# Optimization experiments

Measured on AMD Instinct MI355X. Metric: run time of the kernel, lower is better.

Reference implementation:

```python
import jax, jax.numpy as jnp
import numpy as np

D_MODEL = 1024
N_HEADS = 16
HEAD_DIM = D_MODEL // N_HEADS
B, T = 4, 2048


def setup_inputs() -> dict:
    key = jax.random.key(0)
    k1, k2, k3, k4 = jax.random.split(key, 4)
    x = jax.random.normal(k1, (B, T, D_MODEL), dtype=jnp.float32)
    # bool key-padding mask: True = masked (padded) position
    pad_mask = jax.random.randint(k2, (B, T), 0, 2).astype(jnp.bool_)
    # torch Linear weights: [out_features, in_features], bias=False
    W_qkv = jax.random.normal(k3, (3 * D_MODEL, D_MODEL), dtype=jnp.float32) * (1.0 / np.sqrt(D_MODEL))
    W_proj = jax.random.normal(k4, (D_MODEL, D_MODEL), dtype=jnp.float32) * (1.0 / np.sqrt(D_MODEL))
    return {"x": x, "pad_mask": pad_mask, "W_qkv": W_qkv, "W_proj": W_proj}


def reference(x, pad_mask, W_qkv, W_proj):
    Bv, Tv, C = x.shape
    H, Dh = N_HEADS, HEAD_DIM
    # qkv projection: x @ W_qkv.T -> [B,T,3C], reshape to [B,T,3,H,Dh]
    qkv = jnp.einsum('btc,oc->bto', x, W_qkv).reshape(Bv, Tv, 3, H, Dh)
    q = jnp.transpose(qkv[:, :, 0], (0, 2, 1, 3))  # [B,H,T,Dh]
    k = jnp.transpose(qkv[:, :, 1], (0, 2, 1, 3))
    v = jnp.transpose(qkv[:, :, 2], (0, 2, 1, 3))
    scale = 1.0 / jnp.sqrt(jnp.asarray(Dh, x.dtype))
    attn = jnp.einsum('bhqd,bhkd->bhqk', q, k) * scale  # [B,H,T,T]
    # key-padding mask: broadcast [B,1,1,T]
    attn = jnp.where(pad_mask[:, None, None, :], -jnp.inf, attn)
    attn = jax.nn.softmax(attn, axis=-1)
    out = jnp.einsum('bhqk,bhkd->bhqd', attn, v)  # [B,H,T,Dh]
    out = jnp.transpose(out, (0, 2, 1, 3)).reshape(Bv, Tv, C)
    return jnp.einsum('btc,oc->bto', out, W_proj)
```

## Files before the change

### kernel.cpp

```cpp
#include <hip/hip_runtime.h>
#include <hip/hip_bf16.h>
#include <stdint.h>

typedef __bf16 bf16_t;
typedef __bf16 bf16x8 __attribute__((ext_vector_type(8)));
typedef __bf16 bf16x4 __attribute__((ext_vector_type(4)));
typedef float f32x4 __attribute__((ext_vector_type(4)));

#define DEVFN static __device__ __forceinline__

DEVFN f32x4 mfma16(bf16x8 a, bf16x8 b, f32x4 c) {
  return __builtin_amdgcn_mfma_f32_16x16x32_bf16(a, b, c, 0, 0, 0);
}

#define GLL16(gsrc, ldst) __builtin_amdgcn_global_load_lds( \
    (__attribute__((address_space(1))) void*)(gsrc), \
    (__attribute__((address_space(3))) void*)(ldst), 16, 0, 0)

#define SCALE_Q 0.1803368801111204f

__global__ void prep(const float* __restrict__ x, const float* __restrict__ wqkv,
                     const float* __restrict__ wproj, bf16_t* __restrict__ xb,
                     bf16_t* __restrict__ wqkvb, bf16_t* __restrict__ wprojb,
                     const int* __restrict__ mask, int* __restrict__ tc,
                     int* __restrict__ nk, bf16_t* __restrict__ kb,
                     bf16_t* __restrict__ vtb) {
  const int tid = threadIdx.x;
  if (blockIdx.x < 12288) {
    const int i = blockIdx.x * 256 + tid;
    const float* s;
    bf16_t* d;
    int off;
    if (i < 2097152) { s = x; d = xb; off = i; }
    else if (i < 2097152 + 786432) { s = wqkv; d = wqkvb; off = i - 2097152; }
    else { s = wproj; d = wprojb; off = i - 2883584; }
    f32x4 v = reinterpret_cast<const f32x4*>(s)[off];
    bf16x4 o;
    o[0] = (bf16_t)v[0]; o[1] = (bf16_t)v[1]; o[2] = (bf16_t)v[2]; o[3] = (bf16_t)v[3];
    reinterpret_cast<bf16x4*>(d)[off] = o;
    return;
  }
  const int b = blockIdx.x - 12288;
  const int lane = tid & 63, wv = tid >> 6;
  __shared__ int nk_s;
  const int* mrow = mask + b * 2048;
  if (wv == 0) {
    int base = 0;
    for (int cs = 0; cs < 2048; cs += 64) {
      const int mval = mrow[cs + lane];
      const unsigned long long bal = __ballot(mval == 0);
      const int pre = __popcll(bal & ((1ull << lane) - 1ull));
      if (!mval) tc[b * 2048 + base + pre] = cs + lane;
      base += __popcll(bal);
    }
    if (lane == 0) nk_s = base;
  }
  __syncthreads();
  const int nkb = nk_s;
  if (tid == 0) nk[b] = nkb;
  for (int i = nkb + tid; i < 2048; i += 256) tc[b * 2048 + i] = -1;
  const int ce = (nkb + 63) & ~63;
  for (int hh = wv; hh < 16; hh += 4) {
    const size_t bh = (size_t)(b * 16 + hh);
    for (int r = nkb; r < ce; ++r) {
      kb[(bh * 2048 + r) * 64 + lane] = (bf16_t)0.f;
      vtb[(bh * 64 + lane) * 2048 + r] = (bf16_t)0.f;
    }
  }
}

__global__ __launch_bounds__(512, 2)
void gemm_qkv8(const bf16_t* __restrict__ A, const bf16_t* __restrict__ Bx,
               bf16_t* __restrict__ qb, bf16_t* __restrict__ kb,
               bf16_t* __restrict__ vtb,
               const int* __restrict__ tc, const int* __restrict__ nkp) {
  constexpr int K = 1024;
  constexpr int NT = 16;
  __shared__ alignas(16) unsigned short At[2][256 * 64];
  __shared__ alignas(16) unsigned short Bt[2][256 * 64];
  const int tid = threadIdx.x, lane = tid & 63, w = tid >> 6;
  const int c = lane & 15, g = lane >> 4;
  const int bid = blockIdx.x;
  const int xcd = bid & 7, j = bid >> 3;
  const int my = xcd * 4 + (j & 3), bx = j >> 2;
  const int oBase = bx * 256, mBase = my * 256;
  const int wm = (w >> 2) * 128, wo = (w & 3) * 64;
  const int which = bx >> 2;
  const bool kv = which != 0;
  const int nkb = nkp[mBase >> 11];
  if (kv && (mBase & 2047) >= nkb) return;

  int brow[4];
#pragma unroll
  for (int i = 0; i < 4; ++i) {
    const int r = (i * 8 + w) * 8 + (lane >> 3);
    if (kv) {
      const int t = tc[(mBase >> 11) * 2048 + (mBase & 2047) + r];
      brow[i] = (mBase & ~2047) + (t < 0 ? 0 : t);
    } else {
      brow[i] = mBase + r;
    }
  }

  auto stageA = [&](int k0, int bi, int i) {
    const int cid = (i * 8 + w) * 64 + lane;
    const int r = cid >> 3, ss = (cid & 7) ^ (r & 7);
    GLL16(A + (size_t)(oBase + r) * K + k0 + ss * 8, &At[bi][(i * 8 + w) * 512]);
  };
  auto stageB = [&](int k0, int bi, int i) {
    const int cid = (i * 8 + w) * 64 + lane;
    const int r = cid >> 3, ss = (cid & 7) ^ (r & 7);
    GLL16(Bx + (size_t)brow[i] * K + k0 + ss * 8, &Bt[bi][(i * 8 + w) * 512]);
  };
  auto rdA = [&](int bi, int of, int kc) -> bf16x8 {
    const int rr = wo + of * 16 + c;
    return *reinterpret_cast<const bf16x8*>(&At[bi][rr * 64 + (((kc * 4 + g) ^ (rr & 7)) * 8)]);
  };
  auto rdB = [&](int bi, int mf, int kc) -> bf16x8 {
    const int rr = wm + mf * 16 + c;
    return *reinterpret_cast<const bf16x8*>(&Bt[bi][rr * 64 + (((kc * 4 + g) ^ (rr & 7)) * 8)]);
  };

  f32x4 acc[4][8] = {};

#pragma unroll
  for (int i = 0; i < 4; ++i) { stageA(0, 0, i); stageB(0, 0, i); }
  asm volatile("s_waitcnt vmcnt(0)" ::: "memory");
  __builtin_amdgcn_s_barrier();
  __builtin_amdgcn_sched_barrier(0);

#define PHASE(mf0, STA, STB, EXTRA)                                      \
  {                                                                      \
    bf16x8 b0k0 = rdB(cur, (mf0), 0), b0k1 = rdB(cur, (mf0), 1);         \
    bf16x8 b1k0 = rdB(cur, (mf0) + 1, 0), b1k1 = rdB(cur, (mf0) + 1, 1); \
    if (more) { STA; STB; }                                              \
    __builtin_amdgcn_s_barrier();                                        \
    asm volatile("s_waitcnt lgkmcnt(0)" ::: "memory");                   \
    __builtin_amdgcn_sched_barrier(0);                                   \
    __builtin_amdgcn_s_setprio(1);                                       \
    _Pragma("unroll")                                                    \
    for (int of = 0; of < 4; ++of) {                                     \
      acc[of][(mf0)]     = mfma16(af[of][0], b0k0, acc[of][(mf0)]);      \
      acc[of][(mf0)]     = mfma16(af[of][1], b0k1, acc[of][(mf0)]);      \
      acc[of][(mf0) + 1] = mfma16(af[of][0], b1k0, acc[of][(mf0) + 1]);  \
      acc[of][(mf0) + 1] = mfma16(af[of][1], b1k1, acc[of][(mf0) + 1]);  \
    }                                                                    \
    __builtin_amdgcn_s_setprio(0);                                       \
    EXTRA;                                                               \
    __builtin_amdgcn_s_barrier();                                        \
    __builtin_amdgcn_sched_barrier(0);                                   \
  }

  for (int t = 0; t < NT; ++t) {
    const int cur = t & 1, nxt = cur ^ 1;
    const int k0n = (t + 1) * 64;
    const bool more = t < NT - 1;
    bf16x8 af[4][2];
#pragma unroll
    for (int of = 0; of < 4; ++of) {
      af[of][0] = rdA(cur, of, 0);
      af[of][1] = rdA(cur, of, 1);
    }
    PHASE(0, stageA(k0n, nxt, 0), stageB(k0n, nxt, 0), ;)
    PHASE(2, stageA(k0n, nxt, 1), stageB(k0n, nxt, 1), ;)
    PHASE(4, stageA(k0n, nxt, 2), stageB(k0n, nxt, 2), ;)
    PHASE(6, stageA(k0n, nxt, 3), stageB(k0n, nxt, 3),
          asm volatile("s_waitcnt vmcnt(0)" ::: "memory"))
  }
#undef PHASE

#pragma unroll
  for (int of = 0; of < 4; ++of) {
    const int o0 = oBase + wo + of * 16 + g * 4;
#pragma unroll
    for (int mf = 0; mf < 8; ++mf) {
      const int m = mBase + wm + mf * 16 + c;
      f32x4 v = acc[of][mf];
      if (which == 0) {
        v[0] *= SCALE_Q; v[1] *= SCALE_Q; v[2] *= SCALE_Q; v[3] *= SCALE_Q;
        bf16x4 bv;
        bv[0] = (bf16_t)v[0]; bv[1] = (bf16_t)v[1]; bv[2] = (bf16_t)v[2]; bv[3] = (bf16_t)v[3];
        const int rem = o0 & 1023;
        const int h = rem >> 6, d0 = rem & 63;
        const int b = m >> 11, t = m & 2047;
        *reinterpret_cast<bf16x4*>(qb + (((size_t)(b * 16 + h)) * 2048 + t) * 64 + d0) = bv;
      } else {
        const int i = m & 2047;
        if (i < nkb) {
          bf16x4 bv;
          bv[0] = (bf16_t)v[0]; bv[1] = (bf16_t)v[1]; bv[2] = (bf16_t)v[2]; bv[3] = (bf16_t)v[3];
          const int rem = o0 & 1023;
          const int h = rem >> 6, d0 = rem & 63;
          const int b = m >> 11;
          const size_t bh = (size_t)(b * 16 + h);
          if (which == 1) {
            *reinterpret_cast<bf16x4*>(kb + (bh * 2048 + i) * 64 + d0) = bv;
          } else {
#pragma unroll
            for (int jj = 0; jj < 4; ++jj)
              vtb[(bh * 64 + d0 + jj) * 2048 + i] = bv[jj];
          }
        }
      }
    }
  }
}

__global__ __launch_bounds__(256, 2)
void gemm_proj(const bf16_t* __restrict__ A, const bf16_t* __restrict__ Bx,
               float* __restrict__ fout) {
  constexpr int K = 1024;
  __shared__ alignas(16) unsigned short At[128 * 64];
  __shared__ alignas(16) unsigned short Bt[128 * 64];
  const int tid = threadIdx.x;
  const int lane = tid & 63, w = tid >> 6;
  const int c = lane & 15, g = lane >> 4;
  const int oBase = blockIdx.x * 128, mBase = blockIdx.y * 128;
  const int wo = (w >> 1) * 64, wm = (w & 1) * 64;

  f32x4 acc[4][4] = {};

  for (int k0 = 0; k0 < K; k0 += 64) {
#pragma unroll
    for (int i = 0; i < 4; ++i) {
      const int cid = (i * 4 + w) * 64 + lane;
      const int r = cid >> 3;
      const int ss = (cid & 7) ^ (r & 7);
      GLL16(A + (size_t)(oBase + r) * K + k0 + ss * 8, &At[(i * 4 + w) * 512]);
      GLL16(Bx + (size_t)(mBase + r) * K + k0 + ss * 8, &Bt[(i * 4 + w) * 512]);
    }
    __syncthreads();
    bf16x8 af[4][2], bfr[4][2];
#pragma unroll
    for (int f = 0; f < 4; ++f) {
#pragma unroll
      for (int kc = 0; kc < 2; ++kc) {
        const int ra = wo + f * 16 + c;
        af[f][kc] = *reinterpret_cast<const bf16x8*>(&At[ra * 64 + ((kc * 4 + g) ^ (ra & 7)) * 8]);
        const int rb = wm + f * 16 + c;
        bfr[f][kc] = *reinterpret_cast<const bf16x8*>(&Bt[rb * 64 + ((kc * 4 + g) ^ (rb & 7)) * 8]);
      }
    }
    __builtin_amdgcn_s_setprio(1);
#pragma unroll
    for (int of = 0; of < 4; ++of)
#pragma unroll
      for (int mf = 0; mf < 4; ++mf)
#pragma unroll
        for (int kc = 0; kc < 2; ++kc)
          acc[of][mf] = mfma16(af[of][kc], bfr[mf][kc], acc[of][mf]);
    __builtin_amdgcn_s_setprio(0);
    __syncthreads();
  }

#pragma unroll
  for (int of = 0; of < 4; ++of) {
    const int o0 = oBase + wo + of * 16 + g * 4;
#pragma unroll
    for (int mf = 0; mf < 4; ++mf) {
      const int m = mBase + wm + mf * 16 + c;
      *reinterpret_cast<f32x4*>(fout + (size_t)m * 1024 + o0) = acc[of][mf];
    }
  }
}

__global__ __launch_bounds__(256, 2)
void attn_fwd(const bf16_t* __restrict__ Qg, const bf16_t* __restrict__ Kg,
              const bf16_t* __restrict__ Vtg, const int* __restrict__ nkp,
              bf16_t* __restrict__ aout) {
  constexpr int T = 2048;
  __shared__ alignas(16) unsigned short KtL[2][64 * 64];
  __shared__ alignas(16) unsigned short VtL[2][64 * 64];
  const int tid = threadIdx.x, lane = tid & 63, w = tid >> 6;
  const int c = lane & 15, g = lane >> 4;
  const int bid = blockIdx.x;
  const int xcd = bid & 7, jj = bid >> 3;
  const int bh = xcd * 8 + (jj & 7), qp = jj >> 3;
  const int b = bh >> 4, h = bh & 15;
  const bf16_t* Qh = Qg + (size_t)bh * T * 64;
  const bf16_t* Kh = Kg + (size_t)bh * T * 64;
  const bf16_t* Vh = Vtg + (size_t)bh * 64 * T;
  const int q0 = qp * 256 + w * 64;
  const int nkb = nkp[b];
  const int ntiles = (nkb + 63) >> 6;

  bf16x8 qfr[4][2];
#pragma unroll
  for (int qq = 0; qq < 4; ++qq)
#pragma unroll
    for (int dc = 0; dc < 2; ++dc)
      qfr[qq][dc] = *reinterpret_cast<const bf16x8*>(
          Qh + (size_t)(q0 + qq * 16 + c) * 64 + dc * 32 + g * 8);

  bf16x8 ones;
#pragma unroll
  for (int i = 0; i < 8; ++i) ones[i] = (bf16_t)1.0f;

  f32x4 oacc[4][4] = {};
  float lrun[4] = {0.f, 0.f, 0.f, 0.f};

  auto stage = [&](int t, int bi) {
    const int kt0 = t * 64;
#pragma unroll
    for (int i = 0; i < 2; ++i) {
      const int cid = (i * 4 + w) * 64 + lane;
      const int r = cid >> 3, p = cid & 7;
      const int lk = p ^ ((r & 3) | (((r >> 3) & 1) << 2));
      GLL16(Kh + (size_t)(kt0 + r) * 64 + lk * 8, &KtL[bi][(i * 4 + w) * 512]);
      const int lv = p ^ (r & 7);
      GLL16(Vh + (size_t)r * T + kt0 + lv * 8, &VtL[bi][(i * 4 + w) * 512]);
    }
  };

  stage(0, 0);
  __syncthreads();

  const int fK = (c & 3) | (((c >> 2) & 1) << 2);

  for (int t = 0; t < ntiles; ++t) {
    const int cur = t & 1;
    if (t + 1 < ntiles) stage(t + 1, cur ^ 1);

    bf16x8 kfr[4][2];
#pragma unroll
    for (int kr = 0; kr < 4; ++kr) {
      const int row = (c >> 2) * 8 + (kr & 1) * 4 + (c & 3) + (kr >> 1) * 32;
#pragma unroll
      for (int dc = 0; dc < 2; ++dc)
        kfr[kr][dc] = *reinterpret_cast<const bf16x8*>(
            &KtL[cur][row * 64 + (((dc * 4 + g) ^ fK) * 8)]);
    }

    const bool tail = (t == ntiles - 1) && (nkb & 63) != 0;
    f32x4 bias4[4];
#pragma unroll
    for (int kr = 0; kr < 4; ++kr) {
      if (tail) {
        const int kbase = t * 64 + g * 8 + (kr & 1) * 4 + (kr >> 1) * 32;
#pragma unroll
        for (int j = 0; j < 4; ++j) bias4[kr][j] = (kbase + j < nkb) ? 0.f : -1e30f;
      } else {
        bias4[kr][0] = bias4[kr][1] = bias4[kr][2] = bias4[kr][3] = 0.f;
      }
    }

    bf16x8 pfr[4][2];
#pragma unroll
    for (int qq = 0; qq < 4; ++qq) {
      f32x4 stq[4];
      __builtin_amdgcn_s_setprio(1);
#pragma unroll
      for (int kr = 0; kr < 4; ++kr) {
        f32x4 z = mfma16(kfr[kr][0], qfr[qq][0], bias4[kr]);
        stq[kr] = mfma16(kfr[kr][1], qfr[qq][1], z);
      }
      __builtin_amdgcn_s_setprio(0);
#pragma unroll
      for (int kc = 0; kc < 2; ++kc) {
        bf16x8 p;
#pragma unroll
        for (int j = 0; j < 4; ++j) {
          p[j]     = (bf16_t)__builtin_amdgcn_exp2f(stq[kc * 2 + 0][j]);
          p[4 + j] = (bf16_t)__builtin_amdgcn_exp2f(stq[kc * 2 + 1][j]);
        }
        pfr[qq][kc] = p;
      }
      f32x4 su = {0.f, 0.f, 0.f, 0.f};
      su = mfma16(ones, pfr[qq][0], su);
      su = mfma16(ones, pfr[qq][1], su);
      lrun[qq] += su[0];
    }

    __builtin_amdgcn_s_setprio(1);
#pragma unroll
    for (int df = 0; df < 4; ++df) {
      bf16x8 va[2];
#pragma unroll
      for (int kc = 0; kc < 2; ++kc) {
        const int r = df * 16 + c;
        va[kc] = *reinterpret_cast<const bf16x8*>(
            &VtL[cur][r * 64 + ((kc * 4 + g) ^ (r & 7)) * 8]);
      }
#pragma unroll
      for (int qq = 0; qq < 4; ++qq)
#pragma unroll
        for (int kc = 0; kc < 2; ++kc)
          oacc[df][qq] = mfma16(va[kc], pfr[qq][kc], oacc[df][qq]);
    }
    __builtin_amdgcn_s_setprio(0);
    __syncthreads();
  }

#pragma unroll
  for (int qq = 0; qq < 4; ++qq) {
    const float inv = 1.0f / lrun[qq];
    const int q = q0 + qq * 16 + c;
#pragma unroll
    for (int df = 0; df < 4; ++df) {
      bf16x4 bv;
#pragma unroll
      for (int j = 0; j < 4; ++j) bv[j] = (bf16_t)(oacc[df][qq][j] * inv);
      const int d0 = df * 16 + g * 4;
      *reinterpret_cast<bf16x4*>(aout + ((size_t)(b * 2048 + q)) * 1024 + h * 64 + d0) = bv;
    }
  }
}

extern "C" void kernel_launch(void* const* d_in, const int* in_sizes, int n_in,
                              void* d_out, int out_size, void* d_ws, size_t ws_size,
                              hipStream_t stream) {
  (void)in_sizes; (void)n_in; (void)out_size; (void)ws_size;
  const float* x = (const float*)d_in[0];
  const int* pmask = (const int*)d_in[1];
  const float* wqkv = (const float*)d_in[2];
  const float* wproj = (const float*)d_in[3];
  float* out = (float*)d_out;
  char* ws = (char*)d_ws;

  bf16_t* xb    = (bf16_t*)(ws + 0);
  bf16_t* aob   = (bf16_t*)(ws + 0);
  bf16_t* wqkvb = (bf16_t*)(ws + 16777216);
  bf16_t* wprojb= (bf16_t*)(ws + 23068672);
  bf16_t* Qb    = (bf16_t*)(ws + 25165824);
  bf16_t* Kb    = (bf16_t*)(ws + 41943040);
  bf16_t* Vtb   = (bf16_t*)(ws + 58720256);

  int* tc  = (int*)d_out;
  int* nkp = tc + 4 * 2048;

  prep<<<12292, 256, 0, stream>>>(x, wqkv, wproj, xb, wqkvb, wprojb,
                                  pmask, tc, nkp, Kb, Vtb);

  gemm_qkv8<<<384, 512, 0, stream>>>(wqkvb, xb, Qb, Kb, Vtb, tc, nkp);
  attn_fwd<<<512, 256, 0, stream>>>(Qb, Kb, Vtb, nkp, aob);
  gemm_proj<<<dim3(8, 64), 256, 0, stream>>>(wprojb, aob, out);
}
```

Baseline: 170.3 us.

## Triple-buffer QKV GEMM with smaller 128x256 tiles and more blocks

The QKV projection GEMM moves from a 256x256 double-buffered tile to a 128(out)x256(token) tile with a three-stage LDS ring. Loads run two k-steps ahead and are throttled with vmcnt(6) waits. The grid doubles to 768 blocks and uses a plain row-major block mapping in place of the XCD-aware swizzle. The goal is to hide global-load latency better and balance work across CUs, at the cost of lower per-block reuse, more total A/B traffic, and weaker L2 locality without the swizzle.

```diff
diff --git a/kernel.cpp b/kernel.cpp
--- a/kernel.cpp
+++ b/kernel.cpp
@@ -69,23 +69,22 @@
   }
 }
 
-__global__ __launch_bounds__(512, 2)
-void gemm_qkv8(const bf16_t* __restrict__ A, const bf16_t* __restrict__ Bx,
+__global__ __launch_bounds__(512, 1)
+void gemm_qkv3(const bf16_t* __restrict__ A, const bf16_t* __restrict__ Bx,
                bf16_t* __restrict__ qb, bf16_t* __restrict__ kb,
                bf16_t* __restrict__ vtb,
                const int* __restrict__ tc, const int* __restrict__ nkp) {
   constexpr int K = 1024;
   constexpr int NT = 16;
-  __shared__ alignas(16) unsigned short At[2][256 * 64];
-  __shared__ alignas(16) unsigned short Bt[2][256 * 64];
+  __shared__ alignas(16) unsigned short At[3][128 * 64];
+  __shared__ alignas(16) unsigned short Bt[3][256 * 64];
   const int tid = threadIdx.x, lane = tid & 63, w = tid >> 6;
   const int c = lane & 15, g = lane >> 4;
   const int bid = blockIdx.x;
-  const int xcd = bid & 7, j = bid >> 3;
-  const int my = xcd * 4 + (j & 3), bx = j >> 2;
-  const int oBase = bx * 256, mBase = my * 256;
-  const int wm = (w >> 2) * 128, wo = (w & 3) * 64;
-  const int which = bx >> 2;
+  const int bx = bid % 24, my = bid / 24;
+  const int oBase = bx * 128, mBase = my * 256;
+  const int wo = (w & 1) * 64, wm = (w >> 1) * 64;
+  const int which = bx >> 3;
   const bool kv = which != 0;
   const int nkb = nkp[mBase >> 11];
   if (kv && (mBase & 2047) >= nkb) return;
@@ -121,59 +120,81 @@
     return *reinterpret_cast<const bf16x8*>(&Bt[bi][rr * 64 + (((kc * 4 + g) ^ (rr & 7)) * 8)]);
   };
 
-  f32x4 acc[4][8] = {};
-
-#pragma unroll
-  for (int i = 0; i < 4; ++i) { stageA(0, 0, i); stageB(0, 0, i); }
-  asm volatile("s_waitcnt vmcnt(0)" ::: "memory");
+  f32x4 acc[4][4] = {};
+
+#pragma unroll
+  for (int i = 0; i < 2; ++i) stageA(0, 0, i);
+#pragma unroll
+  for (int i = 0; i < 4; ++i) stageB(0, 0, i);
+#pragma unroll
+  for (int i = 0; i < 2; ++i) stageA(64, 1, i);
+#pragma unroll
+  for (int i = 0; i < 4; ++i) stageB(64, 1, i);
+  asm volatile("s_waitcnt vmcnt(6)" ::: "memory");
   __builtin_amdgcn_s_barrier();
   __builtin_amdgcn_sched_barrier(0);
 
-#define PHASE(mf0, STA, STB, EXTRA)                                      \
-  {                                                                      \
-    bf16x8 b0k0 = rdB(cur, (mf0), 0), b0k1 = rdB(cur, (mf0), 1);         \
-    bf16x8 b1k0 = rdB(cur, (mf0) + 1, 0), b1k1 = rdB(cur, (mf0) + 1, 1); \
-    if (more) { STA; STB; }                                              \
-    __builtin_amdgcn_s_barrier();                                        \
-    asm volatile("s_waitcnt lgkmcnt(0)" ::: "memory");                   \
-    __builtin_amdgcn_sched_barrier(0);                                   \
-    __builtin_amdgcn_s_setprio(1);                                       \
-    _Pragma("unroll")                                                    \
-    for (int of = 0; of < 4; ++of) {                                     \
-      acc[of][(mf0)]     = mfma16(af[of][0], b0k0, acc[of][(mf0)]);      \
-      acc[of][(mf0)]     = mfma16(af[of][1], b0k1, acc[of][(mf0)]);      \
-      acc[of][(mf0) + 1] = mfma16(af[of][0], b1k0, acc[of][(mf0) + 1]);  \
-      acc[of][(mf0) + 1] = mfma16(af[of][1], b1k1, acc[of][(mf0) + 1]);  \
-    }                                                                    \
-    __builtin_amdgcn_s_setprio(0);                                       \
-    EXTRA;                                                               \
-    __builtin_amdgcn_s_barrier();                                        \
-    __builtin_amdgcn_sched_barrier(0);                                   \
-  }
-
+  int bi = 0;
   for (int t = 0; t < NT; ++t) {
-    const int cur = t & 1, nxt = cur ^ 1;
-    const int k0n = (t + 1) * 64;
-    const bool more = t < NT - 1;
+    const int bi2 = (t + 2 < 3) ? (t + 2) : ((t + 2) % 3);
+    const int k2 = (t + 2) * 64;
+    const bool more2 = (t + 2) < NT;
+
     bf16x8 af[4][2];
 #pragma unroll
     for (int of = 0; of < 4; ++of) {
-      af[of][0] = rdA(cur, of, 0);
-      af[of][1] = rdA(cur, of, 1);
-    }
-    PHASE(0, stageA(k0n, nxt, 0), stageB(k0n, nxt, 0), ;)
-    PHASE(2, stageA(k0n, nxt, 1), stageB(k0n, nxt, 1), ;)
-    PHASE(4, stageA(k0n, nxt, 2), stageB(k0n, nxt, 2), ;)
-    PHASE(6, stageA(k0n, nxt, 3), stageB(k0n, nxt, 3),
-          asm volatile("s_waitcnt vmcnt(0)" ::: "memory"))
-  }
-#undef PHASE
+      af[of][0] = rdA(bi, of, 0);
+      af[of][1] = rdA(bi, of, 1);
+    }
+    bf16x8 b00 = rdB(bi, 0, 0), b01 = rdB(bi, 0, 1);
+    bf16x8 b10 = rdB(bi, 1, 0), b11 = rdB(bi, 1, 1);
+    if (more2) { stageA(k2, bi2, 0); stageA(k2, bi2, 1); stageB(k2, bi2, 0); }
+    __builtin_amdgcn_s_barrier();
+    asm volatile("s_waitcnt lgkmcnt(0)" ::: "memory");
+    __builtin_amdgcn_sched_barrier(0);
+    __builtin_amdgcn_s_setprio(1);
+#pragma unroll
+    for (int of = 0; of < 4; ++of) {
+      acc[of][0] = mfma16(af[of][0], b00, acc[of][0]);
+      acc[of][0] = mfma16(af[of][1], b01, acc[of][0]);
+      acc[of][1] = mfma16(af[of][0], b10, acc[of][1]);
+      acc[of][1] = mfma16(af[of][1], b11, acc[of][1]);
+    }
+    __builtin_amdgcn_s_setprio(0);
+    __builtin_amdgcn_s_barrier();
+    __builtin_amdgcn_sched_barrier(0);
+
+    bf16x8 b20 = rdB(bi, 2, 0), b21 = rdB(bi, 2, 1);
+    bf16x8 b30 = rdB(bi, 3, 0), b31 = rdB(bi, 3, 1);
+    if (more2) { stageB(k2, bi2, 1); stageB(k2, bi2, 2); stageB(k2, bi2, 3); }
+    __builtin_amdgcn_s_barrier();
+    asm volatile("s_waitcnt lgkmcnt(0)" ::: "memory");
+    __builtin_amdgcn_sched_barrier(0);
+    __builtin_amdgcn_s_setprio(1);
+#pragma unroll
+    for (int of = 0; of < 4; ++of) {
+      acc[of][2] = mfma16(af[of][0], b20, acc[of][2]);
+      acc[of][2] = mfma16(af[of][1], b21, acc[of][2]);
+      acc[of][3] = mfma16(af[of][0], b30, acc[of][3]);
+      acc[of][3] = mfma16(af[of][1], b31, acc[of][3]);
+    }
+    __builtin_amdgcn_s_setprio(0);
+    if (t < NT - 2) {
+      asm volatile("s_waitcnt vmcnt(6)" ::: "memory");
+    } else if (t == NT - 2) {
+      asm volatile("s_waitcnt vmcnt(0)" ::: "memory");
+    }
+    __builtin_amdgcn_s_barrier();
+    __builtin_amdgcn_sched_barrier(0);
+
+    bi = (bi == 2) ? 0 : bi + 1;
+  }
 
 #pragma unroll
   for (int of = 0; of < 4; ++of) {
     const int o0 = oBase + wo + of * 16 + g * 4;
 #pragma unroll
-    for (int mf = 0; mf < 8; ++mf) {
+    for (int mf = 0; mf < 4; ++mf) {
       const int m = mBase + wm + mf * 16 + c;
       f32x4 v = acc[of][mf];
       if (which == 0) {
@@ -431,7 +452,7 @@
   prep<<<12292, 256, 0, stream>>>(x, wqkv, wproj, xb, wqkvb, wprojb,
                                   pmask, tc, nkp, Kb, Vtb);
 
-  gemm_qkv8<<<384, 512, 0, stream>>>(wqkvb, xb, Qb, Kb, Vtb, tc, nkp);
+  gemm_qkv3<<<768, 512, 0, stream>>>(wqkvb, xb, Qb, Kb, Vtb, tc, nkp);
   attn_fwd<<<512, 256, 0, stream>>>(Qb, Kb, Vtb, nkp, aob);
   gemm_proj<<<dim3(8, 64), 256, 0, stream>>>(wprojb, aob, out);
 }
```

Result: faster. 165.9 us (-2.6%).
